# Optimization experiments

Measured on AMD Instinct MI355X. Metric: run time of the kernel, lower is better.

The kernel has to match this reference:

```python
import jax, jax.numpy as jnp
import numpy as np

D_MODEL = 2048
NUM_HEADS = 32
NUM_KV_HEADS = 8
D_K = D_MODEL // NUM_HEADS
BATCH = 2
SEQ = 2048


def setup_inputs() -> dict:
    key = jax.random.key(0)
    ks = jax.random.split(key, 9)
    s_in = 1.0 / np.sqrt(D_MODEL)
    kv_dim = NUM_KV_HEADS * D_K
    return {
        "x": jax.random.normal(ks[0], (BATCH, SEQ, D_MODEL), jnp.float32),
        "Wq": jax.random.uniform(ks[1], (D_MODEL, D_MODEL), jnp.float32, -s_in, s_in),
        "bq": jax.random.uniform(ks[2], (D_MODEL,), jnp.float32, -s_in, s_in),
        "Wk": jax.random.uniform(ks[3], (D_MODEL, kv_dim), jnp.float32, -s_in, s_in),
        "bk": jax.random.uniform(ks[4], (kv_dim,), jnp.float32, -s_in, s_in),
        "Wv": jax.random.uniform(ks[5], (D_MODEL, kv_dim), jnp.float32, -s_in, s_in),
        "bv": jax.random.uniform(ks[6], (kv_dim,), jnp.float32, -s_in, s_in),
        "Wo": jax.random.uniform(ks[7], (D_MODEL, D_MODEL), jnp.float32, -s_in, s_in),
        "bo": jax.random.uniform(ks[8], (D_MODEL,), jnp.float32, -s_in, s_in),
    }


def reference(x, Wq, bq, Wk, bk, Wv, bv, Wo, bo):
    b, s, _ = x.shape
    rep = NUM_HEADS // NUM_KV_HEADS
    # projections
    q = (x @ Wq + bq).reshape(b, s, NUM_HEADS, D_K).transpose(0, 2, 1, 3)      # [b,h,s,d]
    k = (x @ Wk + bk).reshape(b, s, NUM_KV_HEADS, D_K).transpose(0, 2, 1, 3)   # [b,g,s,d]
    v = (x @ Wv + bv).reshape(b, s, NUM_KV_HEADS, D_K).transpose(0, 2, 1, 3)
    # repeat_interleave over kv heads (head h uses kv head h // rep)
    k = jnp.repeat(k, rep, axis=1)  # [b,h,s,d]
    v = jnp.repeat(v, rep, axis=1)
    scale = 1.0 / np.sqrt(D_K).astype(np.float32)
    scores = jnp.einsum("bhqd,bhkd->bhqk", q, k) * scale
    probs = jax.nn.softmax(scores, axis=-1)
    ctx = jnp.einsum("bhqk,bhkd->bhqd", probs, v)        # [b,h,s,d]
    ctx = ctx.transpose(0, 2, 1, 3).reshape(b, s, D_MODEL)
    return ctx @ Wo + bo
```

## Files before the change

### kernel.cpp

```cpp
#include <hip/hip_runtime.h>
#include <hip/hip_bf16.h>
#include <cstdint>

#define D_MODEL 2048
#define NHEADS 32
#define NKV 8
#define DK 64
#define BATCH 2
#define SEQ 2048
#define M_TOT (BATCH * SEQ)
#define KV_DIM (NKV * DK)
#define QSCALE 0.18033688011112042f
#define MSUB 20.0f

typedef __attribute__((ext_vector_type(8))) short short8;
typedef __attribute__((ext_vector_type(4))) short short4_;
typedef __attribute__((ext_vector_type(2))) float f32x2;
typedef __attribute__((ext_vector_type(4))) float f32x4;
typedef __attribute__((ext_vector_type(16))) float f32x16;
typedef unsigned short u16;
typedef unsigned int u32;

__device__ __forceinline__ u16 f2bf(float f) {
  u32 u = __builtin_bit_cast(u32, f);
  u += 0x7fffu + ((u >> 16) & 1u);
  return (u16)(u >> 16);
}

__device__ __forceinline__ u32 cvtpk(float a, float b) {
  u32 r;
  asm("v_cvt_pk_bf16_f32 %0, %1, %2" : "=v"(r) : "v"(a), "v"(b));
  return r;
}

__device__ __forceinline__ float exp2v(float x) {
  float r;
  asm("v_exp_f32 %0, %1" : "=v"(r) : "v"(x));
  return r;
}

__device__ __forceinline__ f32x2 pkadd(f32x2 a, f32x2 b) {
  f32x2 r;
  asm("v_pk_add_f32 %0, %1, %2" : "=v"(r) : "v"(a), "v"(b));
  return r;
}

__device__ __forceinline__ void gld_lds16(const u16* g, u16* l) {
  __builtin_amdgcn_global_load_lds((__attribute__((address_space(1))) void*)g,
                                   (__attribute__((address_space(3))) void*)l,
                                   16, 0, 0);
}

__global__ void k_convert(const float* __restrict__ in, u16* __restrict__ out, int n4) {
  int i = blockIdx.x * blockDim.x + threadIdx.x;
  if (i >= n4) return;
  float4 v = reinterpret_cast<const float4*>(in)[i];
  uint2 o;
  o.x = (u32)f2bf(v.x) | ((u32)f2bf(v.y) << 16);
  o.y = (u32)f2bf(v.z) | ((u32)f2bf(v.w) << 16);
  reinterpret_cast<uint2*>(out)[i] = o;
}

__global__ void k_transpose(const float* __restrict__ W, u16* __restrict__ Wt,
                            int K, int N) {
  __shared__ float tile[32][33];
  int n0 = blockIdx.x * 32, k0 = blockIdx.y * 32;
  int tx = threadIdx.x, ty = threadIdx.y;
#pragma unroll
  for (int j = 0; j < 4; ++j)
    tile[ty + j * 8][tx] = W[(size_t)(k0 + ty + j * 8) * N + n0 + tx];
  __syncthreads();
#pragma unroll
  for (int j = 0; j < 4; ++j)
    Wt[(size_t)(n0 + ty + j * 8) * K + k0 + tx] = f2bf(tile[tx][ty + j * 8]);
}

template <int MODE, int NBX, int NWG>
__global__ __launch_bounds__(256, 4) void k_gemm128(
    const u16* __restrict__ A, const u16* __restrict__ Bt,
    const float* __restrict__ b0, const float* __restrict__ b1,
    const float* __restrict__ b2,
    u16* __restrict__ O0, u16* __restrict__ O1, u16* __restrict__ O2,
    float* __restrict__ Of) {
  __shared__ u16 Alds[2][128 * 32];
  __shared__ u16 Blds[2][128 * 32];
  const int tid = threadIdx.x;
  const int lane = tid & 63;
  const int wid = tid >> 6;
  const int wr = wid >> 1, wc = wid & 1;
  const int l15 = lane & 15, lg = lane >> 4;
  const int bid = blockIdx.x;
  const int swz = (bid & 7) * (NWG / 8) + (bid >> 3);
  const int by = swz / NBX, bx = swz % NBX;
  const int row0 = by * 128, col0 = bx * 128;

  const u16* pa0 = A  + (size_t)(row0 + (tid >> 2)) * D_MODEL + (tid & 3) * 8;
  const u16* pa1 = pa0 + (size_t)64 * D_MODEL;
  const u16* pb0 = Bt + (size_t)(col0 + (tid >> 2)) * D_MODEL + (tid & 3) * 8;
  const u16* pb1 = pb0 + (size_t)64 * D_MODEL;

  f32x4 acc[4][4];
#pragma unroll
  for (int m = 0; m < 4; ++m)
#pragma unroll
    for (int n = 0; n < 4; ++n) acc[m][n] = (f32x4){0.f, 0.f, 0.f, 0.f};

#define GSTAGE(CUR, KOFF) do {                                                 \
  gld_lds16(pa0 + (KOFF), &Alds[CUR][tid * 8]);                                \
  gld_lds16(pa1 + (KOFF), &Alds[CUR][(tid + 256) * 8]);                        \
  gld_lds16(pb0 + (KOFF), &Blds[CUR][tid * 8]);                                \
  gld_lds16(pb1 + (KOFF), &Blds[CUR][(tid + 256) * 8]);                        \
} while (0)

#define GCOMPUTE(CUR) do {                                                     \
  short8 af_[4], bf_[4];                                                       \
  _Pragma("unroll")                                                            \
  for (int m = 0; m < 4; ++m)                                                  \
    af_[m] = *(const short8*)(&Alds[CUR][(wr * 64 + m * 16 + l15) * 32 + lg * 8]); \
  _Pragma("unroll")                                                            \
  for (int n = 0; n < 4; ++n)                                                  \
    bf_[n] = *(const short8*)(&Blds[CUR][(wc * 64 + n * 16 + l15) * 32 + lg * 8]); \
  _Pragma("unroll")                                                            \
  for (int m = 0; m < 4; ++m)                                                  \
    _Pragma("unroll")                                                          \
    for (int n = 0; n < 4; ++n)                                                \
      acc[m][n] = __builtin_amdgcn_mfma_f32_16x16x32_bf16(af_[m], bf_[n], acc[m][n], 0, 0, 0); \
} while (0)

  GSTAGE(0, 0);
  for (int kt = 0; kt < 64; kt += 2) {
    __syncthreads();
    if (kt + 1 < 64) GSTAGE(1, (kt + 1) * 32);
    GCOMPUTE(0);
    __syncthreads();
    if (kt + 2 < 64) GSTAGE(0, (kt + 2) * 32);
    GCOMPUTE(1);
  }
#undef GSTAGE
#undef GCOMPUTE

  if (MODE == 1) {
#pragma unroll
    for (int m = 0; m < 4; ++m)
#pragma unroll
      for (int n = 0; n < 4; ++n) {
        int col = col0 + wc * 64 + n * 16 + l15;
        float bb = b0[col];
#pragma unroll
        for (int j = 0; j < 4; ++j) {
          int row = row0 + wr * 64 + m * 16 + lg * 4 + j;
          Of[(size_t)row * D_MODEL + col] = acc[m][n][j] + bb;
        }
      }
  } else if (col0 < 2048) {
#pragma unroll
    for (int m = 0; m < 4; ++m)
#pragma unroll
      for (int n = 0; n < 4; ++n) {
        int col = col0 + wc * 64 + n * 16 + l15;
        float bb = b0[col];
#pragma unroll
        for (int j = 0; j < 4; ++j) {
          int row = row0 + wr * 64 + m * 16 + lg * 4 + j;
          O0[(size_t)row * D_MODEL + col] = f2bf((acc[m][n][j] + bb) * QSCALE);
        }
      }
  } else if (col0 < 2560) {
#pragma unroll
    for (int m = 0; m < 4; ++m)
#pragma unroll
      for (int n = 0; n < 4; ++n) {
        int ck = col0 - 2048 + wc * 64 + n * 16 + l15;
        float bb = b1[ck];
#pragma unroll
        for (int j = 0; j < 4; ++j) {
          int row = row0 + wr * 64 + m * 16 + lg * 4 + j;
          O1[(size_t)row * KV_DIM + ck] = f2bf(acc[m][n][j] + bb);
        }
      }
  } else {
#pragma unroll
    for (int m = 0; m < 4; ++m)
#pragma unroll
      for (int n = 0; n < 4; ++n) {
        int dv = col0 - 2560 + wc * 64 + n * 16 + l15;
        float bb = b2[dv];
        int rowb = row0 + wr * 64 + m * 16 + lg * 4;
        short4_ w;
#pragma unroll
        for (int j = 0; j < 4; ++j) w[j] = (short)f2bf(acc[m][n][j] + bb);
        *(short4_*)(O2 + (size_t)dv * M_TOT + rowb) = w;
      }
  }
}

__global__ __launch_bounds__(512) void k_attn(
    const u16* __restrict__ Qb, const u16* __restrict__ Kb,
    const u16* __restrict__ Vt, u16* __restrict__ Ctx) {
  __shared__ u16 smem[4 * 4096];
  const int tid = threadIdx.x;
  const int lane = tid & 63;
  const int wid = tid >> 6;
  const int l31 = lane & 31;
  const int hi = lane >> 5;
  const bool ishi = hi != 0;
  const int b = blockIdx.z, h = blockIdx.y, g = h >> 2;
  const int qrow = blockIdx.x * 256 + wid * 32 + l31;
  const size_t tok = (size_t)b * SEQ + qrow;

  short8 qf[4];
  const u16* qp = Qb + tok * D_MODEL + h * DK + hi * 8;
#pragma unroll
  for (int d = 0; d < 4; ++d) qf[d] = *(const short8*)(qp + d * 16);

  f32x16 oacc0, oacc1;
#pragma unroll
  for (int i = 0; i < 16; ++i) { oacc0[i] = 0.f; oacc1[i] = 0.f; }
  float lrun = 0.f;

  char* sm = (char*)smem;
  const u16* Ksrc = Kb + (size_t)b * SEQ * KV_DIM + g * DK;
  const u16* Vsrc = Vt + (size_t)g * DK * M_TOT + b * SEQ;

#define STAGE(CUR, KV0) do {                                                   \
  int r_ = tid >> 3, c_ = tid & 7, cg_ = c_ ^ (r_ & 7);                        \
  gld_lds16(Ksrc + (size_t)((KV0) + r_) * KV_DIM + cg_ * 8,                    \
            smem + (CUR) * 4096 + tid * 8);                                    \
  gld_lds16(Vsrc + (size_t)r_ * M_TOT + (KV0) + cg_ * 8,                       \
            smem + 8192 + (CUR) * 4096 + tid * 8);                             \
} while (0)

  STAGE(0, 0);

  for (int t = 0; t < SEQ / 64; ++t) {
    const int cur = t & 1;
    __syncthreads();
    if (t + 1 < SEQ / 64) STAGE(cur ^ 1, (t + 1) * 64);

    f32x16 sacc0, sacc1;
#pragma unroll
    for (int i = 0; i < 16; ++i) { sacc0[i] = 0.f; sacc1[i] = 0.f; }
    const char* kbase = sm + cur * 8192;
    const int r0 = l31, r1 = 32 + l31;
    __builtin_amdgcn_s_setprio(1);
#pragma unroll
    for (int d = 0; d < 4; ++d) {
      short8 k0 = *(const short8*)(kbase + r0 * 128 + (((d * 2 + hi) ^ (r0 & 7)) * 16));
      short8 k1 = *(const short8*)(kbase + r1 * 128 + (((d * 2 + hi) ^ (r1 & 7)) * 16));
      sacc0 = __builtin_amdgcn_mfma_f32_32x32x16_bf16(k0, qf[d], sacc0, 0, 0, 0);
      sacc1 = __builtin_amdgcn_mfma_f32_32x32x16_bf16(k1, qf[d], sacc1, 0, 0, 0);
    }
    __builtin_amdgcn_s_setprio(0);

    float pe0[16], pe1[16];
    f32x2 sum2 = (f32x2){0.f, 0.f};
    const f32x2 negM = (f32x2){-MSUB, -MSUB};
#pragma unroll
    for (int i = 0; i < 8; ++i) {
      f32x2 a0 = pkadd((f32x2){sacc0[2 * i], sacc0[2 * i + 1]}, negM);
      f32x2 a1 = pkadd((f32x2){sacc1[2 * i], sacc1[2 * i + 1]}, negM);
      pe0[2 * i] = exp2v(a0[0]);
      pe0[2 * i + 1] = exp2v(a0[1]);
      pe1[2 * i] = exp2v(a1[0]);
      pe1[2 * i + 1] = exp2v(a1[1]);
      sum2 = pkadd(sum2, (f32x2){pe0[2 * i], pe0[2 * i + 1]});
      sum2 = pkadd(sum2, (f32x2){pe1[2 * i], pe1[2 * i + 1]});
    }
    float s32 = sum2[0] + sum2[1];
    s32 += __shfl_xor(s32, 32);
    lrun += s32;

    const char* vbase = sm + 16384 + cur * 8192;

#define PV_STEP(PE, RB, KB) do {                                               \
  u32 A_ = cvtpk(PE[(RB) + 0], PE[(RB) + 1]);                                  \
  u32 B_ = cvtpk(PE[(RB) + 4], PE[(RB) + 5]);                                  \
  u32 C_ = cvtpk(PE[(RB) + 2], PE[(RB) + 3]);                                  \
  u32 E_ = cvtpk(PE[(RB) + 6], PE[(RB) + 7]);                                  \
  u32 Ax_ = __shfl_xor(A_, 32), Bx_ = __shfl_xor(B_, 32);                      \
  u32 Cx_ = __shfl_xor(C_, 32), Ex_ = __shfl_xor(E_, 32);                      \
  union { u32 w[4]; short8 s8; } uu_;                                          \
  uu_.w[0] = ishi ? Bx_ : A_;                                                  \
  uu_.w[1] = ishi ? Ex_ : C_;                                                  \
  uu_.w[2] = ishi ? B_ : Ax_;                                                  \
  uu_.w[3] = ishi ? E_ : Cx_;                                                  \
  short8 pf_ = uu_.s8;                                                         \
  short8 vf0_ = *(const short8*)(vbase + r0 * 128 + ((((KB) * 2 + hi) ^ (r0 & 7)) * 16)); \
  short8 vf1_ = *(const short8*)(vbase + r1 * 128 + ((((KB) * 2 + hi) ^ (r1 & 7)) * 16)); \
  __builtin_amdgcn_s_setprio(1);                                               \
  oacc0 = __builtin_amdgcn_mfma_f32_32x32x16_bf16(vf0_, pf_, oacc0, 0, 0, 0);  \
  oacc1 = __builtin_amdgcn_mfma_f32_32x32x16_bf16(vf1_, pf_, oacc1, 0, 0, 0);  \
  __builtin_amdgcn_s_setprio(0);                                               \
} while (0)

    PV_STEP(pe0, 0, 0);
    PV_STEP(pe0, 8, 1);
    PV_STEP(pe1, 0, 2);
    PV_STEP(pe1, 8, 3);
#undef PV_STEP
  }

  float rl = 1.0f / lrun;
  u16* cp = Ctx + tok * D_MODEL + h * DK;
#pragma unroll
  for (int db = 0; db < 2; ++db) {
    const f32x16& oa = db ? oacc1 : oacc0;
#pragma unroll
    for (int quad = 0; quad < 4; ++quad) {
      int dbase = db * 32 + 8 * quad + 4 * hi;
      short4_ w;
#pragma unroll
      for (int j = 0; j < 4; ++j) w[j] = (short)f2bf(oa[quad * 4 + j] * rl);
      *(short4_*)(cp + dbase) = w;
    }
  }
#undef STAGE
}

extern "C" void kernel_launch(void* const* d_in, const int* in_sizes, int n_in,
                              void* d_out, int out_size, void* d_ws, size_t ws_size,
                              hipStream_t stream) {
  const float* x  = (const float*)d_in[0];
  const float* Wq = (const float*)d_in[1];
  const float* bq = (const float*)d_in[2];
  const float* Wk = (const float*)d_in[3];
  const float* bk = (const float*)d_in[4];
  const float* Wv = (const float*)d_in[5];
  const float* bv = (const float*)d_in[6];
  const float* Wo = (const float*)d_in[7];
  const float* bo = (const float*)d_in[8];
  float* out = (float*)d_out;

  char* ws = (char*)d_ws;
  u16* xb    = (u16*)(ws);
  u16* Wqkvt = (u16*)(ws + 16777216);
  u16* Wot   = (u16*)(ws + 29360128);
  u16* Qb    = (u16*)(ws + 37748736);
  u16* Kb    = (u16*)(ws + 54525952);
  u16* Vtr   = (u16*)(ws + 58720256);
  u16* Ctx   = (u16*)(ws + 62914560);

  int n4 = M_TOT * D_MODEL / 4;
  k_convert<<<(n4 + 255) / 256, 256, 0, stream>>>(x, xb, n4);
  k_transpose<<<dim3(64, 64), dim3(32, 8), 0, stream>>>(Wq, Wqkvt, D_MODEL, D_MODEL);
  k_transpose<<<dim3(16, 64), dim3(32, 8), 0, stream>>>(Wk, Wqkvt + (size_t)2048 * D_MODEL, D_MODEL, KV_DIM);
  k_transpose<<<dim3(16, 64), dim3(32, 8), 0, stream>>>(Wv, Wqkvt + (size_t)2560 * D_MODEL, D_MODEL, KV_DIM);
  k_transpose<<<dim3(64, 64), dim3(32, 8), 0, stream>>>(Wo, Wot, D_MODEL, D_MODEL);

  k_gemm128<0, 24, 768><<<768, 256, 0, stream>>>(xb, Wqkvt, bq, bk, bv, Qb, Kb, Vtr, nullptr);

  k_attn<<<dim3(SEQ / 256, NHEADS, BATCH), 512, 0, stream>>>(Qb, Kb, Vtr, Ctx);

  k_gemm128<1, 16, 512><<<512, 256, 0, stream>>>(Ctx, Wot, bo, nullptr, nullptr,
                                                 nullptr, nullptr, nullptr, out);
}
```

Before: 225.9 us.

## Triple-buffer K/V staging in attention and use permlane32 swaps for P exchange

Switches the attention kernel's K/V LDS staging from double to triple buffering, prefetching two tiles ahead and synchronising with explicit vmcnt waits plus a raw barrier instead of __syncthreads. It also replaces the __shfl_xor lane exchanges (ds_bpermute through LDS) for the P operand and the row-sum reduction with v_permlane32_swap, which removes the select logic. The aim is to hide global-load latency and cut LDS traffic in the inner loop. The cost is 50% more shared memory per block, which could lower occupancy.

```diff
diff --git a/kernel.cpp b/kernel.cpp
--- a/kernel.cpp
+++ b/kernel.cpp
@@ -197,13 +197,12 @@
 __global__ __launch_bounds__(512) void k_attn(
     const u16* __restrict__ Qb, const u16* __restrict__ Kb,
     const u16* __restrict__ Vt, u16* __restrict__ Ctx) {
-  __shared__ u16 smem[4 * 4096];
+  __shared__ u16 smem[6 * 4096];
   const int tid = threadIdx.x;
   const int lane = tid & 63;
   const int wid = tid >> 6;
   const int l31 = lane & 31;
   const int hi = lane >> 5;
-  const bool ishi = hi != 0;
   const int b = blockIdx.z, h = blockIdx.y, g = h >> 2;
   const int qrow = blockIdx.x * 256 + wid * 32 + l31;
   const size_t tok = (size_t)b * SEQ + qrow;
@@ -227,21 +226,36 @@
   gld_lds16(Ksrc + (size_t)((KV0) + r_) * KV_DIM + cg_ * 8,                    \
             smem + (CUR) * 4096 + tid * 8);                                    \
   gld_lds16(Vsrc + (size_t)r_ * M_TOT + (KV0) + cg_ * 8,                       \
-            smem + 8192 + (CUR) * 4096 + tid * 8);                             \
+            smem + 12288 + (CUR) * 4096 + tid * 8);                            \
 } while (0)
 
   STAGE(0, 0);
-
-  for (int t = 0; t < SEQ / 64; ++t) {
-    const int cur = t & 1;
-    __syncthreads();
-    if (t + 1 < SEQ / 64) STAGE(cur ^ 1, (t + 1) * 64);
+  STAGE(1, 64);
+
+  int cur = 0;
+  const int r0 = l31, r1 = 32 + l31;
+
+#pragma unroll 1
+  for (int t = 0; t < 32; ++t) {
+    if (t < 31) {
+      asm volatile("s_waitcnt vmcnt(2)" ::: "memory");
+    } else {
+      asm volatile("s_waitcnt vmcnt(0)" ::: "memory");
+    }
+    __builtin_amdgcn_s_barrier();
+    __builtin_amdgcn_sched_barrier(0);
+
+    if (t + 2 < 32) {
+      int nx = cur + 2; if (nx >= 3) nx -= 3;
+      STAGE(nx, (t + 2) * 64);
+    }
+
+    const char* kbase = sm + cur * 8192;
+    const char* vbase = sm + 24576 + cur * 8192;
 
     f32x16 sacc0, sacc1;
 #pragma unroll
     for (int i = 0; i < 16; ++i) { sacc0[i] = 0.f; sacc1[i] = 0.f; }
-    const char* kbase = sm + cur * 8192;
-    const int r0 = l31, r1 = 32 + l31;
     __builtin_amdgcn_s_setprio(1);
 #pragma unroll
     for (int d = 0; d < 4; ++d) {
@@ -253,7 +267,7 @@
     __builtin_amdgcn_s_setprio(0);
 
     float pe0[16], pe1[16];
-    f32x2 sum2 = (f32x2){0.f, 0.f};
+    f32x2 sA = (f32x2){0.f, 0.f}, sB = (f32x2){0.f, 0.f};
     const f32x2 negM = (f32x2){-MSUB, -MSUB};
 #pragma unroll
     for (int i = 0; i < 8; ++i) {
@@ -263,27 +277,25 @@
       pe0[2 * i + 1] = exp2v(a0[1]);
       pe1[2 * i] = exp2v(a1[0]);
       pe1[2 * i + 1] = exp2v(a1[1]);
-      sum2 = pkadd(sum2, (f32x2){pe0[2 * i], pe0[2 * i + 1]});
-      sum2 = pkadd(sum2, (f32x2){pe1[2 * i], pe1[2 * i + 1]});
-    }
-    float s32 = sum2[0] + sum2[1];
-    s32 += __shfl_xor(s32, 32);
-    lrun += s32;
-
-    const char* vbase = sm + 16384 + cur * 8192;
+      sA = pkadd(sA, (f32x2){pe0[2 * i], pe0[2 * i + 1]});
+      sB = pkadd(sB, (f32x2){pe1[2 * i], pe1[2 * i + 1]});
+    }
+    float s32 = (sA[0] + sA[1]) + (sB[0] + sB[1]);
+    {
+      u32 xs = __builtin_bit_cast(u32, s32), ys = xs;
+      asm volatile("v_permlane32_swap_b32 %0, %1" : "+v"(xs), "+v"(ys));
+      lrun += __builtin_bit_cast(float, xs) + __builtin_bit_cast(float, ys);
+    }
 
 #define PV_STEP(PE, RB, KB) do {                                               \
-  u32 A_ = cvtpk(PE[(RB) + 0], PE[(RB) + 1]);                                  \
-  u32 B_ = cvtpk(PE[(RB) + 4], PE[(RB) + 5]);                                  \
-  u32 C_ = cvtpk(PE[(RB) + 2], PE[(RB) + 3]);                                  \
-  u32 E_ = cvtpk(PE[(RB) + 6], PE[(RB) + 7]);                                  \
-  u32 Ax_ = __shfl_xor(A_, 32), Bx_ = __shfl_xor(B_, 32);                      \
-  u32 Cx_ = __shfl_xor(C_, 32), Ex_ = __shfl_xor(E_, 32);                      \
+  u32 w0_ = cvtpk(PE[(RB) + 0], PE[(RB) + 1]);                                 \
+  u32 w1_ = cvtpk(PE[(RB) + 2], PE[(RB) + 3]);                                 \
+  u32 w2_ = cvtpk(PE[(RB) + 4], PE[(RB) + 5]);                                 \
+  u32 w3_ = cvtpk(PE[(RB) + 6], PE[(RB) + 7]);                                 \
+  asm volatile("v_permlane32_swap_b32 %0, %1" : "+v"(w0_), "+v"(w2_));         \
+  asm volatile("v_permlane32_swap_b32 %0, %1" : "+v"(w1_), "+v"(w3_));         \
   union { u32 w[4]; short8 s8; } uu_;                                          \
-  uu_.w[0] = ishi ? Bx_ : A_;                                                  \
-  uu_.w[1] = ishi ? Ex_ : C_;                                                  \
-  uu_.w[2] = ishi ? B_ : Ax_;                                                  \
-  uu_.w[3] = ishi ? E_ : Cx_;                                                  \
+  uu_.w[0] = w0_; uu_.w[1] = w1_; uu_.w[2] = w2_; uu_.w[3] = w3_;              \
   short8 pf_ = uu_.s8;                                                         \
   short8 vf0_ = *(const short8*)(vbase + r0 * 128 + ((((KB) * 2 + hi) ^ (r0 & 7)) * 16)); \
   short8 vf1_ = *(const short8*)(vbase + r1 * 128 + ((((KB) * 2 + hi) ^ (r1 & 7)) * 16)); \
@@ -298,6 +310,8 @@
     PV_STEP(pe1, 0, 2);
     PV_STEP(pe1, 8, 3);
 #undef PV_STEP
+
+    ++cur; if (cur == 3) cur = 0;
   }
 
   float rl = 1.0f / lrun;
```

Result: faster. 220.1 us (-2.6%).
